# Performance work log

Hardware: AMD Instinct MI355X
Metric: run time of the kernel (lower is better)

Reference implementation:

```python
import jax, jax.numpy as jnp
import numpy as np

N = 1024  # batch rows; each row has 480 features

def setup_inputs() -> dict:
    key = jax.random.key(0)
    kx, kS, kT, kH, kL = jax.random.split(key, 5)
    x = jax.random.normal(kx, (N, 480), dtype=jnp.float32)
    S = jax.random.normal(kS, (30, 2, 15), dtype=jnp.float32)    # buffer
    T = jax.random.normal(kT, (30, 15), dtype=jnp.float32)       # param
    H = jax.random.normal(kH, (45, 4096), dtype=jnp.float32)     # buffer (hash matrix)
    LUT = jax.random.normal(kL, (10, 4096, 2), dtype=jnp.float32)  # param (codebook)
    return {"x": x, "S": S, "T": T, "H": H, "LUT": LUT}

def reference(x, S, T, H, LUT):
    # (N, 480) -> (N, 8, 30, 2)
    x4 = x.reshape(-1, 8, 30, 2)
    # project each 2-vector through S: (N, 8, 30, 15)
    y = jnp.einsum('abcd,cdk->abck', x4, S) - T - 1e-4
    # straight-through sign-tanh binarization
    tanh = jnp.tanh(y)
    y = jax.lax.stop_gradient(jnp.sign(y) - tanh) + tanh
    # (N, 8, 10, 45): 30*15 = 10*(3*15)
    y = y.reshape(-1, 8, 10, 45)
    # hash scores over 4096 codes: (N, 8, 10, 4096)
    scores = jnp.einsum('bpcd,dk->bpck', y, H)
    idx = jnp.argmax(scores, axis=-1)  # (N, 8, 10) int
    # one_hot @ LUT is exactly a gather: out[b,p,c,:] = LUT[c, idx[b,p,c], :]
    out = LUT[jnp.arange(10)[None, None, :], idx]  # (N, 8, 10, 2)
    return out
```

## Files before the change

### kernel.cpp

```cpp
#include <hip/hip_runtime.h>
#include <math.h>

#define M_ROWS  81920
#define NCOLS   4096
#define KPAD    48
#define NCHUNK  4
#define CHUNKC  (NCOLS / NCHUNK)
#define CROUNDS (CHUNKC / 32)
#define GROUNDS (NCOLS / 32)
#define FRAG    512
#define ROUND6  (6 * FRAG)
#define LO_SCALE 4096.0f

typedef _Float16 f16x8  __attribute__((ext_vector_type(8)));
typedef float    f32x16 __attribute__((ext_vector_type(16)));


__global__ void build_B_kernel(const float* __restrict__ H,
                               _Float16* __restrict__ B_pk) {
    const int n = blockIdx.x * 256 + threadIdx.x;
    const int r = n >> 5;
    const int l = n & 31;
    float hi[KPAD], lo[KPAD];
    #pragma unroll
    for (int k = 0; k < 45; ++k) {
        const float h = H[k * NCOLS + n];
        const _Float16 h1 = (_Float16)h;
        hi[k] = (float)h1 * LO_SCALE;
        lo[k] = (h - (float)h1) * LO_SCALE;
    }
    #pragma unroll
    for (int k = 45; k < KPAD; ++k) { hi[k] = 0.f; lo[k] = 0.f; }
    _Float16* dst = B_pk + (size_t)r * ROUND6;
    #pragma unroll
    for (int kt = 0; kt < 3; ++kt) {
        f16x8 l0, l1v, h0, h1v;
        #pragma unroll
        for (int j = 0; j < 8; ++j) {
            l0[j]  = (_Float16)lo[kt * 16 + j];
            l1v[j] = (_Float16)lo[kt * 16 + 8 + j];
            h0[j]  = (_Float16)hi[kt * 16 + j];
            h1v[j] = (_Float16)hi[kt * 16 + 8 + j];
        }
        *(f16x8*)(dst + kt * FRAG + l * 8)              = l0;
        *(f16x8*)(dst + kt * FRAG + (l + 32) * 8)       = l1v;
        *(f16x8*)(dst + (3 + kt) * FRAG + l * 8)        = h0;
        *(f16x8*)(dst + (3 + kt) * FRAG + (l + 32) * 8) = h1v;
    }
}

__global__ __launch_bounds__(256, 2) void score_argmax_kernel(
        const float* __restrict__ x,
        const float* __restrict__ S,
        const float* __restrict__ T,
        const _Float16* __restrict__ B_pk,
        float* __restrict__ pbest,
        int*   __restrict__ pidx) {
    const int tid  = threadIdx.x;
    const int lane = tid & 63;
    const int l31  = lane & 31;
    const int half = lane >> 5;
    const int chunk = blockIdx.x / 320;
    const int rg    = (blockIdx.x - chunk * 320) * 4 + (tid >> 6);
    const int rowbase = rg * 64;

    f16x8 afr[2][3];
    #pragma unroll
    for (int rt = 0; rt < 2; ++rt) {
        const int row  = rowbase + rt * 32 + l31;
        const int pair = row / 10;
        const int c2   = row - pair * 10;
        const int a    = pair >> 3;
        const int b    = pair & 7;
        const float* xp = x + a * 480 + b * 60;
        #pragma unroll
        for (int kt = 0; kt < 3; ++kt) {
            #pragma unroll
            for (int j = 0; j < 8; ++j) {
                const int k    = kt * 16 + half * 8 + j;
                const bool pad = (k >= 45);
                const int kcl  = pad ? 0 : k;
                const int cc   = kcl / 15;
                const int kk   = kcl - cc * 15;
                const int c    = c2 * 3 + cc;
                const float x0 = xp[c * 2 + 0];
                const float x1 = xp[c * 2 + 1];
                float v = x0 * S[(c * 2 + 0) * 15 + kk] + x1 * S[(c * 2 + 1) * 15 + kk];
                v = v - T[c * 15 + kk] - 1e-4f;
                const float yv = (v > 0.f) ? 1.f : ((v < 0.f) ? -1.f : 0.f);
                afr[rt][kt][j] = pad ? (_Float16)0.f : (_Float16)yv;
            }
        }
    }

    float best[2][16];
    int   bidx[2][16];
    #pragma unroll
    for (int rt = 0; rt < 2; ++rt)
        #pragma unroll
        for (int e = 0; e < 16; ++e) { best[rt][e] = -INFINITY; bidx[rt][e] = 0; }

    f32x16 czero;
    #pragma unroll
    for (int e = 0; e < 16; ++e) czero[e] = 0.f;

    const int colbase0 = chunk * CHUNKC;
    const _Float16* bbase = B_pk + (size_t)(chunk * CROUNDS) * ROUND6 + lane * 8;

    for (int ct = 0; ct < CROUNDS; ++ct) {
        const _Float16* bp = bbase + (size_t)ct * ROUND6;
        const f16x8 bl0 = *(const f16x8*)(bp);
        const f16x8 bl1 = *(const f16x8*)(bp + FRAG);
        const f16x8 bl2 = *(const f16x8*)(bp + 2 * FRAG);
        const f16x8 bh0 = *(const f16x8*)(bp + 3 * FRAG);
        const f16x8 bh1 = *(const f16x8*)(bp + 4 * FRAG);
        const f16x8 bh2 = *(const f16x8*)(bp + 5 * FRAG);

        const int mycol = colbase0 + ct * 32 + l31;
        #pragma unroll
        for (int rt = 0; rt < 2; ++rt) {
            f32x16 acc = czero;
            acc = __builtin_amdgcn_mfma_f32_32x32x16_f16(afr[rt][0], bl0, acc, 0, 0, 0);
            acc = __builtin_amdgcn_mfma_f32_32x32x16_f16(afr[rt][1], bl1, acc, 0, 0, 0);
            acc = __builtin_amdgcn_mfma_f32_32x32x16_f16(afr[rt][2], bl2, acc, 0, 0, 0);
            acc = __builtin_amdgcn_mfma_f32_32x32x16_f16(afr[rt][0], bh0, acc, 0, 0, 0);
            acc = __builtin_amdgcn_mfma_f32_32x32x16_f16(afr[rt][1], bh1, acc, 0, 0, 0);
            acc = __builtin_amdgcn_mfma_f32_32x32x16_f16(afr[rt][2], bh2, acc, 0, 0, 0);
            #pragma unroll
            for (int e = 0; e < 16; ++e) {
                const float s = acc[e];
                if (s > best[rt][e]) bidx[rt][e] = mycol;
                best[rt][e] = fmaxf(best[rt][e], s);
            }
        }
    }

    #pragma unroll
    for (int m = 1; m < 32; m <<= 1) {
        #pragma unroll
        for (int rt = 0; rt < 2; ++rt)
            #pragma unroll
            for (int e = 0; e < 16; ++e) {
                const float ov = __shfl_xor(best[rt][e], m, 64);
                const int   oi = __shfl_xor(bidx[rt][e], m, 64);
                if (ov > best[rt][e] ||
                    (ov == best[rt][e] && oi < bidx[rt][e])) {
                    best[rt][e] = ov; bidx[rt][e] = oi;
                }
            }
    }

    if (l31 == 0) {
        #pragma unroll
        for (int rt = 0; rt < 2; ++rt)
            #pragma unroll
            for (int e = 0; e < 16; ++e) {
                const int row = rowbase + rt * 32 + (e & 3) + 8 * (e >> 2) + 4 * half;
                pbest[(size_t)row * NCHUNK + chunk] = best[rt][e];
                pidx [(size_t)row * NCHUNK + chunk] = bidx[rt][e];
            }
    }
}

__global__ void reduce_lut_kernel(const float* __restrict__ pbest,
                                  const int*   __restrict__ pidx,
                                  const float* __restrict__ LUT,
                                  float* __restrict__ out) {
    const int row = blockIdx.x * blockDim.x + threadIdx.x;
    if (row >= M_ROWS) return;
    float best = -INFINITY;
    int   bi   = 0;
    #pragma unroll
    for (int ch = 0; ch < NCHUNK; ++ch) {
        const float bv = pbest[(size_t)row * NCHUNK + ch];
        const int   ix = pidx [(size_t)row * NCHUNK + ch];
        if (bv > best) { best = bv; bi = ix; }
    }
    const int pair = row / 10;
    const int c2   = row - pair * 10;
    const float* l = LUT + ((size_t)c2 * NCOLS + bi) * 2;
    out[row * 2 + 0] = l[0];
    out[row * 2 + 1] = l[1];
}

extern "C" void kernel_launch(void* const* d_in, const int* in_sizes, int n_in,
                              void* d_out, int out_size, void* d_ws, size_t ws_size,
                              hipStream_t stream) {
    const float* x   = (const float*)d_in[0];
    const float* S   = (const float*)d_in[1];
    const float* T   = (const float*)d_in[2];
    const float* H   = (const float*)d_in[3];
    const float* LUT = (const float*)d_in[4];
    float* out = (float*)d_out;

    _Float16* B_pk = (_Float16*)d_ws;
    float*  pbest = (float*)(B_pk + (size_t)GROUNDS * ROUND6);
    int*    pidx  = (int*)(pbest + (size_t)M_ROWS * NCHUNK);

    build_B_kernel<<<16, 256, 0, stream>>>(H, B_pk);
    score_argmax_kernel<<<1280, 256, 0, stream>>>(x, S, T, B_pk, pbest, pidx);
    reduce_lut_kernel<<<M_ROWS / 256, 256, 0, stream>>>(pbest, pidx, LUT, out);
}
```

Baseline: 224.5 us.

## Precompute binarized A fragments, stage H chunk in LDS, split columns finer

Moves the sign-binarization of the input rows into a separate kernel that writes packed f16 MFMA fragments. Each score block now converts its 256-column slice of H into hi/lo f16 fragments directly in shared memory and reads B from LDS instead of a global buffer. The column dimension is split into 16 chunks instead of 4, giving 5120 blocks. The hi and lo MFMA chains use separate accumulators for more instruction-level parallelism. The trade-offs are that every block redoes the H conversion, and the partial-result buffers and final reduction grow fourfold.

```diff
diff --git a/kernel.cpp b/kernel.cpp
--- a/kernel.cpp
+++ b/kernel.cpp
@@ -4,10 +4,9 @@
 #define M_ROWS  81920
 #define NCOLS   4096
 #define KPAD    48
-#define NCHUNK  4
+#define NCHUNK  16
 #define CHUNKC  (NCOLS / NCHUNK)
 #define CROUNDS (CHUNKC / 32)
-#define GROUNDS (NCOLS / 32)
 #define FRAG    512
 #define ROUND6  (6 * FRAG)
 #define LO_SCALE 4096.0f
@@ -16,82 +15,101 @@
 typedef float    f32x16 __attribute__((ext_vector_type(16)));
 
 
-__global__ void build_B_kernel(const float* __restrict__ H,
-                               _Float16* __restrict__ B_pk) {
-    const int n = blockIdx.x * 256 + threadIdx.x;
-    const int r = n >> 5;
-    const int l = n & 31;
-    float hi[KPAD], lo[KPAD];
-    #pragma unroll
-    for (int k = 0; k < 45; ++k) {
-        const float h = H[k * NCOLS + n];
-        const _Float16 h1 = (_Float16)h;
-        hi[k] = (float)h1 * LO_SCALE;
-        lo[k] = (h - (float)h1) * LO_SCALE;
-    }
-    #pragma unroll
-    for (int k = 45; k < KPAD; ++k) { hi[k] = 0.f; lo[k] = 0.f; }
-    _Float16* dst = B_pk + (size_t)r * ROUND6;
+__global__ void build_A_kernel(const float* __restrict__ x,
+                               const float* __restrict__ S,
+                               const float* __restrict__ T,
+                               _Float16* __restrict__ A_pk) {
+    const int row  = blockIdx.x * 256 + threadIdx.x;
+    const int pair = row / 10;
+    const int c2   = row - pair * 10;
+    const int a    = pair >> 3;
+    const int b    = pair & 7;
+    const float* xp = x + a * 480 + b * 60;
+    _Float16 y[KPAD];
+    #pragma unroll
+    for (int j = 0; j < 45; ++j) {
+        const int c = c2 * 3 + j / 15;
+        const int k = j % 15;
+        const float x0 = xp[c * 2 + 0];
+        const float x1 = xp[c * 2 + 1];
+        float v = x0 * S[(c * 2 + 0) * 15 + k] + x1 * S[(c * 2 + 1) * 15 + k];
+        v = v - T[c * 15 + k] - 1e-4f;
+        y[j] = (v > 0.f) ? (_Float16)1.f : ((v < 0.f) ? (_Float16)-1.f : (_Float16)0.f);
+    }
+    #pragma unroll
+    for (int j = 45; j < KPAD; ++j) y[j] = (_Float16)0.f;
+
+    const int rg32 = row >> 5;
+    const int l    = row & 31;
     #pragma unroll
     for (int kt = 0; kt < 3; ++kt) {
-        f16x8 l0, l1v, h0, h1v;
-        #pragma unroll
-        for (int j = 0; j < 8; ++j) {
-            l0[j]  = (_Float16)lo[kt * 16 + j];
-            l1v[j] = (_Float16)lo[kt * 16 + 8 + j];
-            h0[j]  = (_Float16)hi[kt * 16 + j];
-            h1v[j] = (_Float16)hi[kt * 16 + 8 + j];
-        }
-        *(f16x8*)(dst + kt * FRAG + l * 8)              = l0;
-        *(f16x8*)(dst + kt * FRAG + (l + 32) * 8)       = l1v;
-        *(f16x8*)(dst + (3 + kt) * FRAG + l * 8)        = h0;
-        *(f16x8*)(dst + (3 + kt) * FRAG + (l + 32) * 8) = h1v;
-    }
-}
-
-__global__ __launch_bounds__(256, 2) void score_argmax_kernel(
-        const float* __restrict__ x,
-        const float* __restrict__ S,
-        const float* __restrict__ T,
-        const _Float16* __restrict__ B_pk,
+        #pragma unroll
+        for (int half = 0; half < 2; ++half) {
+            f16x8 fr;
+            #pragma unroll
+            for (int j = 0; j < 8; ++j) fr[j] = y[kt * 16 + half * 8 + j];
+            *(f16x8*)(A_pk + ((size_t)rg32 * 3 + kt) * FRAG + (half * 32 + l) * 8) = fr;
+        }
+    }
+}
+
+__global__ __launch_bounds__(256) void score_argmax_kernel(
+        const float* __restrict__ H,
+        const _Float16* __restrict__ A_pk,
         float* __restrict__ pbest,
         int*   __restrict__ pidx) {
-    const int tid  = threadIdx.x;
+    __shared__ _Float16 lds[CROUNDS * ROUND6];
+
+    const int tid   = threadIdx.x;
+    const int chunk = blockIdx.x / 320;
+    const int local = blockIdx.x - chunk * 320;
+
+    {
+        const int r = tid >> 5;
+        const int l = tid & 31;
+        const int n = chunk * CHUNKC + r * 32 + l;
+        float hi[KPAD], lo[KPAD];
+        #pragma unroll
+        for (int k = 0; k < 45; ++k) {
+            const float h = H[k * NCOLS + n];
+            const _Float16 h1 = (_Float16)h;
+            hi[k] = (float)h1 * LO_SCALE;
+            lo[k] = (h - (float)h1) * LO_SCALE;
+        }
+        #pragma unroll
+        for (int k = 45; k < KPAD; ++k) { hi[k] = 0.f; lo[k] = 0.f; }
+        _Float16* dst = lds + (size_t)r * ROUND6;
+        #pragma unroll
+        for (int kt = 0; kt < 3; ++kt) {
+            f16x8 l0, l1v, h0, h1v;
+            #pragma unroll
+            for (int j = 0; j < 8; ++j) {
+                l0[j]  = (_Float16)lo[kt * 16 + j];
+                l1v[j] = (_Float16)lo[kt * 16 + 8 + j];
+                h0[j]  = (_Float16)hi[kt * 16 + j];
+                h1v[j] = (_Float16)hi[kt * 16 + 8 + j];
+            }
+            *(f16x8*)(dst + kt * FRAG + l * 8)              = l0;
+            *(f16x8*)(dst + kt * FRAG + (l + 32) * 8)       = l1v;
+            *(f16x8*)(dst + (3 + kt) * FRAG + l * 8)        = h0;
+            *(f16x8*)(dst + (3 + kt) * FRAG + (l + 32) * 8) = h1v;
+        }
+    }
+    __syncthreads();
+
     const int lane = tid & 63;
     const int l31  = lane & 31;
     const int half = lane >> 5;
-    const int chunk = blockIdx.x / 320;
-    const int rg    = (blockIdx.x - chunk * 320) * 4 + (tid >> 6);
+    const int rg   = local * 4 + (tid >> 6);
     const int rowbase = rg * 64;
 
     f16x8 afr[2][3];
     #pragma unroll
-    for (int rt = 0; rt < 2; ++rt) {
-        const int row  = rowbase + rt * 32 + l31;
-        const int pair = row / 10;
-        const int c2   = row - pair * 10;
-        const int a    = pair >> 3;
-        const int b    = pair & 7;
-        const float* xp = x + a * 480 + b * 60;
-        #pragma unroll
-        for (int kt = 0; kt < 3; ++kt) {
-            #pragma unroll
-            for (int j = 0; j < 8; ++j) {
-                const int k    = kt * 16 + half * 8 + j;
-                const bool pad = (k >= 45);
-                const int kcl  = pad ? 0 : k;
-                const int cc   = kcl / 15;
-                const int kk   = kcl - cc * 15;
-                const int c    = c2 * 3 + cc;
-                const float x0 = xp[c * 2 + 0];
-                const float x1 = xp[c * 2 + 1];
-                float v = x0 * S[(c * 2 + 0) * 15 + kk] + x1 * S[(c * 2 + 1) * 15 + kk];
-                v = v - T[c * 15 + kk] - 1e-4f;
-                const float yv = (v > 0.f) ? 1.f : ((v < 0.f) ? -1.f : 0.f);
-                afr[rt][kt][j] = pad ? (_Float16)0.f : (_Float16)yv;
-            }
-        }
-    }
+    for (int rt = 0; rt < 2; ++rt)
+        #pragma unroll
+        for (int kt = 0; kt < 3; ++kt)
+            afr[rt][kt] = *(const f16x8*)(A_pk
+                + ((size_t)((rowbase >> 5) + rt) * 3 + kt) * FRAG + lane * 8);
 
     float best[2][16];
     int   bidx[2][16];
@@ -105,7 +123,7 @@
     for (int e = 0; e < 16; ++e) czero[e] = 0.f;
 
     const int colbase0 = chunk * CHUNKC;
-    const _Float16* bbase = B_pk + (size_t)(chunk * CROUNDS) * ROUND6 + lane * 8;
+    const _Float16* bbase = lds + lane * 8;
 
     for (int ct = 0; ct < CROUNDS; ++ct) {
         const _Float16* bp = bbase + (size_t)ct * ROUND6;
@@ -119,16 +137,15 @@
         const int mycol = colbase0 + ct * 32 + l31;
         #pragma unroll
         for (int rt = 0; rt < 2; ++rt) {
-            f32x16 acc = czero;
-            acc = __builtin_amdgcn_mfma_f32_32x32x16_f16(afr[rt][0], bl0, acc, 0, 0, 0);
-            acc = __builtin_amdgcn_mfma_f32_32x32x16_f16(afr[rt][1], bl1, acc, 0, 0, 0);
-            acc = __builtin_amdgcn_mfma_f32_32x32x16_f16(afr[rt][2], bl2, acc, 0, 0, 0);
-            acc = __builtin_amdgcn_mfma_f32_32x32x16_f16(afr[rt][0], bh0, acc, 0, 0, 0);
-            acc = __builtin_amdgcn_mfma_f32_32x32x16_f16(afr[rt][1], bh1, acc, 0, 0, 0);
-            acc = __builtin_amdgcn_mfma_f32_32x32x16_f16(afr[rt][2], bh2, acc, 0, 0, 0);
+            f32x16 cl = __builtin_amdgcn_mfma_f32_32x32x16_f16(afr[rt][0], bl0, czero, 0, 0, 0);
+            f32x16 ch = __builtin_amdgcn_mfma_f32_32x32x16_f16(afr[rt][0], bh0, czero, 0, 0, 0);
+            cl = __builtin_amdgcn_mfma_f32_32x32x16_f16(afr[rt][1], bl1, cl, 0, 0, 0);
+            ch = __builtin_amdgcn_mfma_f32_32x32x16_f16(afr[rt][1], bh1, ch, 0, 0, 0);
+            cl = __builtin_amdgcn_mfma_f32_32x32x16_f16(afr[rt][2], bl2, cl, 0, 0, 0);
+            ch = __builtin_amdgcn_mfma_f32_32x32x16_f16(afr[rt][2], bh2, ch, 0, 0, 0);
             #pragma unroll
             for (int e = 0; e < 16; ++e) {
-                const float s = acc[e];
+                const float s = ch[e] + cl[e];
                 if (s > best[rt][e]) bidx[rt][e] = mycol;
                 best[rt][e] = fmaxf(best[rt][e], s);
             }
@@ -193,11 +210,11 @@
     const float* LUT = (const float*)d_in[4];
     float* out = (float*)d_out;
 
-    _Float16* B_pk = (_Float16*)d_ws;
-    float*  pbest = (float*)(B_pk + (size_t)GROUNDS * ROUND6);
+    _Float16* A_pk = (_Float16*)d_ws;
+    float*  pbest = (float*)(A_pk + (size_t)2560 * 3 * FRAG);
     int*    pidx  = (int*)(pbest + (size_t)M_ROWS * NCHUNK);
 
-    build_B_kernel<<<16, 256, 0, stream>>>(H, B_pk);
-    score_argmax_kernel<<<1280, 256, 0, stream>>>(x, S, T, B_pk, pbest, pidx);
+    build_A_kernel<<<M_ROWS / 256, 256, 0, stream>>>(x, S, T, A_pk);
+    score_argmax_kernel<<<5120, 256, 0, stream>>>(H, A_pk, pbest, pidx);
     reduce_lut_kernel<<<M_ROWS / 256, 256, 0, stream>>>(pbest, pidx, LUT, out);
 }
```

Result: slower. 293.9 us (+30.9%).
